# Optimization experiments

Hardware: AMD Instinct MI355X
Metric: run time of the kernel (lower is better)

## Reference

```python
import jax, jax.numpy as jnp
import numpy as np

N0, N1, N2 = 200000, 50000, 10000
D_IN, D_PROMPT, D_HID, D_OUT = 128, 64, 256, 2
E0, E1 = 800000, 160000


def _glorot(key, shape):
    fan_in, fan_out = shape[0], shape[1]
    lim = np.sqrt(6.0 / (fan_in + fan_out))
    return jax.random.uniform(key, shape, jnp.float32, -lim, lim)


def setup_inputs() -> dict:
    key = jax.random.key(0)
    ks = jax.random.split(key, 20)
    inp = {
        "features": jax.random.normal(ks[0], (N0, D_IN), jnp.float32),
        "membership_mask": jax.random.randint(ks[1], (N0,), 0, 2) > 0,
        "src0": jax.random.randint(ks[2], (E0,), 0, N0),
        "dst0": jax.random.randint(ks[3], (E0,), 0, N1),
        "src1": jax.random.randint(ks[4], (E1,), 0, N1),
        "dst1": jax.random.randint(ks[5], (E1,), 0, N2),
        "output_nodes_indices": jax.random.randint(ks[6], (N2,), 0, N2),
        # prompt MLPs
        "w_pin": _glorot(ks[7], (D_IN, D_PROMPT)),
        "b_pin": jnp.zeros((D_PROMPT,), jnp.float32),
        "w_pout": _glorot(ks[8], (D_IN, D_PROMPT)),
        "b_pout": jnp.zeros((D_PROMPT,), jnp.float32),
        # SAGEConv layer 0: (D_IN+D_PROMPT) -> D_HID
        "w_self0": _glorot(ks[9], (D_IN + D_PROMPT, D_HID)),
        "w_neigh0": _glorot(ks[10], (D_IN + D_PROMPT, D_HID)),
        "b0": jnp.zeros((D_HID,), jnp.float32),
        # SAGEConv layer 1: D_HID -> D_HID
        "w_self1": _glorot(ks[11], (D_HID, D_HID)),
        "w_neigh1": _glorot(ks[12], (D_HID, D_HID)),
        "b1": jnp.zeros((D_HID,), jnp.float32),
        # classifier
        "w_cls": _glorot(ks[13], (D_HID, D_OUT)),
        "b_cls": jnp.zeros((D_OUT,), jnp.float32),
    }
    return inp


def _sage_mean(h, src, dst, n_dst, w_self, w_neigh, b):
    # mean-aggregate src features into dst buckets (zero-degree -> 0, DGL semantics)
    agg = jax.ops.segment_sum(h[src], dst, num_segments=n_dst)
    deg = jax.ops.segment_sum(jnp.ones((src.shape[0],), h.dtype), dst, num_segments=n_dst)
    agg = agg / jnp.maximum(deg, 1.0)[:, None]
    return h[:n_dst] @ w_self + agg @ w_neigh + b


def reference(features, membership_mask, src0, dst0, src1, dst1, output_nodes_indices,
              w_pin, b_pin, w_pout, b_pout,
              w_self0, w_neigh0, b0, w_self1, w_neigh1, b1, w_cls, b_cls):
    p_in = jax.nn.relu(features @ w_pin + b_pin)
    p_out = jax.nn.relu(features @ w_pout + b_pout)
    sel = jnp.where(membership_mask[:, None], p_in, p_out)
    h = jnp.concatenate([features, sel], axis=1)          # [N0, D_IN+D_PROMPT]
    h = jax.nn.relu(_sage_mean(h, src0, dst0, N1, w_self0, w_neigh0, b0))  # [N1, D_HID]
    h = _sage_mean(h, src1, dst1, N2, w_self1, w_neigh1, b1)               # [N2, D_HID]
    logits = h @ w_cls + b_cls                             # [N2, D_OUT]
    return logits
```

## Files before the change

kernel.cpp:

```cpp
#include <hip/hip_runtime.h>


#define N0v 200000
#define N1v 50000
#define N2v 10000
#define E0v 800000
#define E1v 160000
#define TB0 49
#define TB1 10
#define TBL (TB0 + TB1)
#define NTILE 3125
#define PGRID 512

using u16 = unsigned short;
typedef __attribute__((ext_vector_type(8))) short short8;
typedef __attribute__((ext_vector_type(4))) float f32x4;

__device__ __forceinline__ float b2f(u16 u) {
    union { unsigned int i; float f; } v; v.i = ((unsigned int)u) << 16; return v.f;
}
__device__ __forceinline__ u16 f2b(float f) {
    union { float f; unsigned int i; } v; v.f = f;
    return (u16)((v.i + 0x7fffu + ((v.i >> 16) & 1u)) >> 16);
}
__device__ __forceinline__ void split2(float f, u16& h, u16& l) {
    h = f2b(f);
    l = f2b(f - b2f(h));
}

__global__ void k_prep(const unsigned* mask, int* flag,
                       const float* w_pin, const float* w_pout, u16* WTph, u16* WTpl,
                       const float* ws0, const float* wn0, u16* WT0h, u16* WT0l,
                       const float* ws1, const float* wn1, u16* WT1h, u16* WT1l,
                       const float* bc, float* outp,
                       const int* __restrict__ dst0, const int* __restrict__ dst1,
                       int* cnt0, int* cnt1, int* rk0, int* rk1) {
    const int R0 = 50000;
    const int R1 = R0 + 128 * 128;
    const int R2 = R1 + 256 * 384;
    const int R3 = R2 + 256 * 512;
    const int R4 = R3 + 2 * N2v;
    const int R5 = R4 + E0v;
    const int R6 = R5 + E1v;
    for (int i = blockIdx.x * blockDim.x + threadIdx.x; i < R6;
         i += gridDim.x * blockDim.x) {
        if (i < R0) {
            if (mask[i] > 1u) atomicOr(flag, 1);
        } else if (i < R1) {
            int j = i - R0, n = j >> 7, k = j & 127;
            float f = (n < 64) ? w_pin[k * 64 + n] : w_pout[k * 64 + (n - 64)];
            split2(f, WTph[j], WTpl[j]);
        } else if (i < R2) {
            int j = i - R1, n = j / 384, k = j % 384;
            float f = (k < 192) ? ws0[k * 256 + n] : wn0[(k - 192) * 256 + n];
            split2(f, WT0h[j], WT0l[j]);
        } else if (i < R3) {
            int j = i - R2, n = j >> 9, k = j & 511;
            float f = (k < 256) ? ws1[k * 256 + n] : wn1[(k - 256) * 256 + n];
            split2(f, WT1h[j], WT1l[j]);
        } else if (i < R4) {
            int j = i - R3;
            outp[j] = bc[j & 1];
        } else if (i < R5) {
            int e = i - R4;
            rk0[e] = atomicAdd(&cnt0[dst0[e]], 1);
        } else {
            int e = i - R5;
            rk1[e] = atomicAdd(&cnt1[dst1[e]], 1);
        }
    }
}

__global__ __launch_bounds__(256) void k_scan_a(const int* __restrict__ cnt0,
                                                int* __restrict__ off0,
                                                const int* __restrict__ cnt1,
                                                int* __restrict__ off1,
                                                int* __restrict__ tsum) {
    __shared__ int sd[256];
    const int t = threadIdx.x;
    const int blk = blockIdx.x;
    const int g1 = (blk >= TB0);
    const int b = g1 ? blk - TB0 : blk;
    const int n = g1 ? N2v : N1v;
    const int* cnt = g1 ? cnt1 : cnt0;
    int* off = g1 ? off1 : off0;
    const int i0 = b * 1024 + t * 4;
    int c[4] = {0, 0, 0, 0};
    if (i0 + 3 < n) {
        *(int4*)c = *(const int4*)&cnt[i0];
    } else {
        for (int j = 0; j < 4; j++) if (i0 + j < n) c[j] = cnt[i0 + j];
    }
    int s = c[0] + c[1] + c[2] + c[3];
    sd[t] = s;
    __syncthreads();
#pragma unroll
    for (int d = 1; d < 256; d <<= 1) {
        int v = (t >= d) ? sd[t - d] : 0;
        __syncthreads();
        sd[t] += v;
        __syncthreads();
    }
    int run = sd[t] - s;
    int o4[4];
#pragma unroll
    for (int j = 0; j < 4; j++) { o4[j] = run; run += c[j]; }
    if (i0 + 3 < n) *(int4*)&off[i0] = *(const int4*)o4;
    else for (int j = 0; j < 4; j++) if (i0 + j < n) off[i0 + j] = o4[j];
    if (t == 255) tsum[blk] = sd[255];
}

__global__ __launch_bounds__(256) void k_scan_c(int* __restrict__ off0,
                                                int* __restrict__ off1,
                                                const int* __restrict__ tsum) {
    __shared__ int lbase;
    const int t = threadIdx.x;
    const int blk = blockIdx.x;
    const int g1 = (blk >= TB0);
    const int b = g1 ? blk - TB0 : blk;
    const int n = g1 ? N2v : N1v;
    int* off = g1 ? off1 : off0;
    if (t < 64) {
        int v = (t < TBL) ? tsum[t] : 0;
        int incl = v;
#pragma unroll
        for (int d = 1; d < 64; d <<= 1) {
            int u = __shfl_up(incl, d);
            if (t >= d) incl += u;
        }
        int total0 = __shfl(incl, TB0 - 1);
        if (t == blk) lbase = (incl - v) - (g1 ? total0 : 0);
    }
    __syncthreads();
    const int base = lbase;
    const int i0 = b * 1024 + t * 4;
    if (i0 + 3 < n) {
        int4 v = *(int4*)&off[i0];
        v.x += base; v.y += base; v.z += base; v.w += base;
        *(int4*)&off[i0] = v;
    } else {
        for (int j = 0; j < 4; j++) if (i0 + j < n) off[i0 + j] += base;
    }
    if (blk == 0 && t == 0) { off0[N1v] = E0v; off1[N2v] = E1v; }
}

__global__ __launch_bounds__(256) void k_scatter2(
    const int* __restrict__ src0, const int* __restrict__ dst0,
    const int* __restrict__ off0, const int* __restrict__ rk0, int* __restrict__ ei0,
    const int* __restrict__ src1, const int* __restrict__ dst1,
    const int* __restrict__ off1, const int* __restrict__ rk1, int* __restrict__ ei1) {
    const int part = blockIdx.x & 7;
    const int chunk = blockIdx.x >> 3;
    const int nch = gridDim.x >> 3;
    {
        const int per = (E0v + nch - 1) / nch;
        const int i1 = min((chunk + 1) * per, E0v);
        for (int i = chunk * per + (int)threadIdx.x; i < i1; i += 256) {
            int d = dst0[i];
            if (d / 6250 == part) ei0[off0[d] + rk0[i]] = src0[i];
        }
    }
    {
        const int per = (E1v + nch - 1) / nch;
        const int i1 = min((chunk + 1) * per, E1v);
        for (int i = chunk * per + (int)threadIdx.x; i < i1; i += 256) {
            int d = dst1[i];
            if (d / 1250 == part) ei1[off1[d] + rk1[i]] = src1[i];
        }
    }
}

__global__ __launch_bounds__(256, 2) void k_gemm_p(
    const float* __restrict__ A, const u16* __restrict__ Bh, const u16* __restrict__ Bl,
    const float* __restrict__ b_pin, const float* __restrict__ b_pout,
    const void* maskp, const int* __restrict__ flag, u16* __restrict__ G) {
    __shared__ __align__(16) u16 STG[2][8448];
    __shared__ __align__(16) u16 EPI[8704];
    const int t = threadIdx.x;
    const int lane = t & 63, w = t >> 6;
    const int m = lane & 15, q = lane >> 4;
    const int colbase = w * 32;
    const int r15 = t >> 4, ch = t & 15;
    const int k0s = ch >> 2, q2s = ch & 3;

    const size_t ba = (size_t)(colbase + m) * 128 + q * 8;
    const size_t bb = (size_t)(colbase + 16 + m) * 128 + q * 8;
    short8 BfA[4][2], BfB[4][2];
#pragma unroll
    for (int k0 = 0; k0 < 4; k0++) {
        BfA[k0][0] = *(const short8*)&Bh[ba + k0 * 32];
        BfA[k0][1] = *(const short8*)&Bl[ba + k0 * 32];
        BfB[k0][0] = *(const short8*)&Bh[bb + k0 * 32];
        BfB[k0][1] = *(const short8*)&Bl[bb + k0 * 32];
    }
    const int fl = *flag;
    float bv0, bv1;
    {
        int c0 = colbase + m, c1 = colbase + 16 + m;
        bv0 = (c0 < 64) ? b_pin[c0] : b_pout[c0 - 64];
        bv1 = (c1 < 64) ? b_pin[c1] : b_pout[c1 - 64];
    }

    float4 va[8];
    {
        const float* ap = &A[(size_t)(blockIdx.x * 64 + r15) * 128 + ch * 8];
#pragma unroll
        for (int p = 0; p < 4; p++) {
            va[2 * p]     = *(const float4*)(ap + (size_t)p * 16 * 128);
            va[2 * p + 1] = *(const float4*)(ap + (size_t)p * 16 * 128 + 4);
        }
    }

    int buf = 0;
    for (int bm = blockIdx.x; bm < NTILE; bm += PGRID, buf ^= 1) {
        const int r0 = bm * 64;
        u16* stg = STG[buf];
#pragma unroll
        for (int p = 0; p < 4; p++) {
            u16 h8[8];
            h8[0] = f2b(va[2 * p].x); h8[1] = f2b(va[2 * p].y);
            h8[2] = f2b(va[2 * p].z); h8[3] = f2b(va[2 * p].w);
            h8[4] = f2b(va[2 * p + 1].x); h8[5] = f2b(va[2 * p + 1].y);
            h8[6] = f2b(va[2 * p + 1].z); h8[7] = f2b(va[2 * p + 1].w);
            *(uint4*)&stg[((p * 4 + k0s) * 66 + 16 * q2s + r15) * 8] = *(const uint4*)h8;
        }
        __syncthreads();

        if (bm + PGRID < NTILE) {
            const float* ap = &A[(size_t)((bm + PGRID) * 64 + r15) * 128 + ch * 8];
#pragma unroll
            for (int p = 0; p < 4; p++) {
                va[2 * p]     = *(const float4*)(ap + (size_t)p * 16 * 128);
                va[2 * p + 1] = *(const float4*)(ap + (size_t)p * 16 * 128 + 4);
            }
        }
        bool mk0, mk1;
        {
            const int ra = r0 + (t >> 3), rb = ra + 32;
            if (fl) {
                mk0 = ((const unsigned char*)maskp)[ra] != 0;
                mk1 = ((const unsigned char*)maskp)[rb] != 0;
            } else {
                mk0 = ((const int*)maskp)[ra] != 0;
                mk1 = ((const int*)maskp)[rb] != 0;
            }
        }

        f32x4 acc[4][2] = {};
#pragma unroll
        for (int k0 = 0; k0 < 4; k0++) {
#pragma unroll
            for (int mi = 0; mi < 4; mi++) {
                short8 af = *(const short8*)&stg[((mi * 4 + k0) * 66 + lane) * 8];
                acc[mi][0] = __builtin_amdgcn_mfma_f32_16x16x32_bf16(af, BfA[k0][0], acc[mi][0], 0, 0, 0);
                acc[mi][0] = __builtin_amdgcn_mfma_f32_16x16x32_bf16(af, BfA[k0][1], acc[mi][0], 0, 0, 0);
                acc[mi][1] = __builtin_amdgcn_mfma_f32_16x16x32_bf16(af, BfB[k0][0], acc[mi][1], 0, 0, 0);
                acc[mi][1] = __builtin_amdgcn_mfma_f32_16x16x32_bf16(af, BfB[k0][1], acc[mi][1], 0, 0, 0);
            }
        }

#pragma unroll
        for (int mi = 0; mi < 4; mi++)
#pragma unroll
            for (int r = 0; r < 4; r++) {
                float v0 = acc[mi][0][r] + bv0;
                float v1 = acc[mi][1][r] + bv1;
                v0 = v0 > 0.f ? v0 : 0.f;
                v1 = v1 > 0.f ? v1 : 0.f;
                EPI[(mi * 16 + q * 4 + r) * 136 + colbase + m] = f2b(v0);
                EPI[(mi * 16 + q * 4 + r) * 136 + colbase + 16 + m] = f2b(v1);
            }
        __syncthreads();

        {
            const int c8 = t & 7;
            const int rt = t >> 3;
            *(uint4*)&G[(size_t)(r0 + rt) * 192 + 128 + c8 * 8] =
                *(const uint4*)&EPI[rt * 136 + (mk0 ? 0 : 64) + c8 * 8];
            *(uint4*)&G[(size_t)(r0 + 32 + rt) * 192 + 128 + c8 * 8] =
                *(const uint4*)&EPI[(32 + rt) * 136 + (mk1 ? 0 : 64) + c8 * 8];
        }
#pragma unroll
        for (int p = 0; p < 4; p++) {
            uint4 v = *(const uint4*)&stg[((p * 4 + k0s) * 66 + 16 * q2s + r15) * 8];
            *(uint4*)&G[(size_t)(r0 + r15 + 16 * p) * 192 + ch * 8] = v;
        }
    }
}

template <int MODE, int KT, int SEGA0, int MT>
__global__ __launch_bounds__(256, 3) void k_g(
    const u16* __restrict__ A0, int s0, const u16* __restrict__ A1, int s1,
    const u16* __restrict__ Bh, const u16* __restrict__ Bl,
    const float* __restrict__ bias,
    u16* __restrict__ CH, float* __restrict__ outp, const float* __restrict__ wc,
    int M) {
    constexpr int MI = MT / 16;
    __shared__ __align__(16) u16 LA[MI * KT * 66 * 8];
    const int t = threadIdx.x;
    const int bm = blockIdx.x >> 1, bn = blockIdx.x & 1;
    const int lane = t & 63, w = t >> 6;
    const int m = lane & 15, q = lane >> 4;
    const int r0 = bm * MT;
    const int colbase = bn * 128 + w * 32;
    const int K = KT * 32;

    {
        constexpr int TPR = 256 / MT;
        constexpr int SPT = KT / TPR;
        const int rr = t / TPR, sub = t & (TPR - 1);
        int arow = r0 + rr; if (arow >= M) arow = M - 1;
        const int mi = rr >> 4, r15 = rr & 15;
#pragma unroll
        for (int s = 0; s < SPT; s++) {
            const int kc = sub * SPT + s;
#pragma unroll
            for (int q2 = 0; q2 < 4; q2++) {
                const int c = kc * 32 + q2 * 8;
                uint4 v = (c < SEGA0)
                              ? *(const uint4*)&A0[(size_t)arow * s0 + c]
                              : *(const uint4*)&A1[(size_t)arow * s1 + (c - SEGA0)];
                *(uint4*)&LA[((mi * KT + kc) * 66 + 16 * q2 + r15) * 8] = v;
            }
        }
    }
    __syncthreads();

    const size_t ba = (size_t)(colbase + m) * K + q * 8;
    const size_t bb = (size_t)(colbase + 16 + m) * K + q * 8;

    f32x4 acc[MI][2] = {};
#pragma unroll 2
    for (int kb = 0; kb < KT; kb += 4) {
#pragma unroll
        for (int k0 = 0; k0 < 4; k0++) {
            const size_t ko = (size_t)(kb + k0) * 32;
            short8 b0h = *(const short8*)&Bh[ba + ko];
            short8 b0l = *(const short8*)&Bl[ba + ko];
            short8 b1h = *(const short8*)&Bh[bb + ko];
            short8 b1l = *(const short8*)&Bl[bb + ko];
#pragma unroll
            for (int mi = 0; mi < MI; mi++) {
                short8 af = *(const short8*)&LA[((mi * KT + kb + k0) * 66 + lane) * 8];
                acc[mi][0] = __builtin_amdgcn_mfma_f32_16x16x32_bf16(af, b0h, acc[mi][0], 0, 0, 0);
                acc[mi][0] = __builtin_amdgcn_mfma_f32_16x16x32_bf16(af, b0l, acc[mi][0], 0, 0, 0);
                acc[mi][1] = __builtin_amdgcn_mfma_f32_16x16x32_bf16(af, b1h, acc[mi][1], 0, 0, 0);
                acc[mi][1] = __builtin_amdgcn_mfma_f32_16x16x32_bf16(af, b1l, acc[mi][1], 0, 0, 0);
            }
        }
    }

    if (MODE == 1) {
        float bv[2];
#pragma unroll
        for (int nt = 0; nt < 2; nt++) bv[nt] = bias[colbase + nt * 16 + m];
        __syncthreads();
#pragma unroll
        for (int mi = 0; mi < MI; mi++)
#pragma unroll
            for (int nt = 0; nt < 2; nt++)
#pragma unroll
                for (int r = 0; r < 4; r++) {
                    float v = acc[mi][nt][r] + bv[nt];
                    v = v > 0.f ? v : 0.f;
                    LA[(mi * 16 + q * 4 + r) * 136 + w * 32 + nt * 16 + m] = f2b(v);
                }
        __syncthreads();
        const int c16 = t & 15;
#pragma unroll
        for (int pass = 0; pass < MT / 16; pass++) {
            const int rt = pass * 16 + (t >> 4);
            const int row = r0 + rt;
            if (row < M) {
                *(uint4*)&CH[(size_t)row * 256 + bn * 128 + c16 * 8] =
                    *(const uint4*)&LA[rt * 136 + c16 * 8];
            }
        }
    } else {
        const int ca = colbase + m, cb = colbase + 16 + m;
        const float bva = bias[ca], bvb = bias[cb];
        const float w0a = wc[ca * 2], w1a = wc[ca * 2 + 1];
        const float w0b = wc[cb * 2], w1b = wc[cb * 2 + 1];
#pragma unroll
        for (int mi = 0; mi < MI; mi++) {
#pragma unroll
            for (int r = 0; r < 4; r++) {
                int row = r0 + mi * 16 + q * 4 + r;
                float va = acc[mi][0][r] + bva;
                float vb = acc[mi][1][r] + bvb;
                float p0 = va * w0a + vb * w0b;
                float p1 = va * w1a + vb * w1b;
#pragma unroll
                for (int s = 1; s < 16; s <<= 1) {
                    p0 += __shfl_xor(p0, s);
                    p1 += __shfl_xor(p1, s);
                }
                if (m == 0 && row < M) {
                    atomicAdd(&outp[row * 2], p0);
                    atomicAdd(&outp[row * 2 + 1], p1);
                }
            }
        }
    }
}

__global__ void k_agg0(const u16* __restrict__ G, const int* __restrict__ off,
                       const int* __restrict__ eidx, u16* __restrict__ aggH) {
    int wid = (blockIdx.x * blockDim.x + threadIdx.x) >> 6;
    int lane = threadIdx.x & 63;
    if (wid >= N1v) return;
    int b = off[wid], e = off[wid + 1];
    float f0 = 0.f, f1 = 0.f, p0 = 0.f;
    for (int base = b; base < e; base += 64) {
        int li = base + lane;
        int idx = eidx[li < e ? li : (e - 1)];
        int nch = e - base; if (nch > 64) nch = 64;
        int j = 0;
        for (; j + 4 <= nch; j += 4) {
            int sa = __shfl(idx, j), sb = __shfl(idx, j + 1);
            int sc = __shfl(idx, j + 2), sd = __shfl(idx, j + 3);
            const u16* ra = &G[(size_t)sa * 192];
            const u16* rb = &G[(size_t)sb * 192];
            const u16* rc = &G[(size_t)sc * 192];
            const u16* rd = &G[(size_t)sd * 192];
            unsigned fa = *(const unsigned*)&ra[2 * lane];
            unsigned fb = *(const unsigned*)&rb[2 * lane];
            unsigned fc = *(const unsigned*)&rc[2 * lane];
            unsigned fd = *(const unsigned*)&rd[2 * lane];
            u16 pa = ra[128 + lane], pb = rb[128 + lane];
            u16 pc = rc[128 + lane], pd = rd[128 + lane];
            f0 += b2f((u16)fa) + b2f((u16)fb) + b2f((u16)fc) + b2f((u16)fd);
            f1 += b2f((u16)(fa >> 16)) + b2f((u16)(fb >> 16)) +
                  b2f((u16)(fc >> 16)) + b2f((u16)(fd >> 16));
            p0 += b2f(pa) + b2f(pb) + b2f(pc) + b2f(pd);
        }
        for (; j < nch; j++) {
            int s = __shfl(idx, j);
            const u16* row = &G[(size_t)s * 192];
            unsigned fv = *(const unsigned*)&row[2 * lane];
            f0 += b2f((u16)fv);
            f1 += b2f((u16)(fv >> 16));
            p0 += b2f(row[128 + lane]);
        }
    }
    int deg = e - b;
    float inv = 1.0f / (float)(deg > 1 ? deg : 1);
    size_t rb2 = (size_t)wid * 192;
    *(unsigned*)&aggH[rb2 + 2 * lane] =
        (unsigned)f2b(f0 * inv) | ((unsigned)f2b(f1 * inv) << 16);
    aggH[rb2 + 128 + lane] = f2b(p0 * inv);
}

__global__ void k_agg1(const u16* __restrict__ h1H, const int* __restrict__ off,
                       const int* __restrict__ eidx, u16* __restrict__ aggH) {
    int wid = (blockIdx.x * blockDim.x + threadIdx.x) >> 6;
    int lane = threadIdx.x & 63;
    if (wid >= N2v) return;
    int b = off[wid], e = off[wid + 1];
    float a0 = 0.f, a1 = 0.f, a2 = 0.f, a3 = 0.f;
    for (int base = b; base < e; base += 64) {
        int li = base + lane;
        int idx = eidx[li < e ? li : (e - 1)];
        int nch = e - base; if (nch > 64) nch = 64;
        int j = 0;
        for (; j + 4 <= nch; j += 4) {
            int sa = __shfl(idx, j), sb = __shfl(idx, j + 1);
            int sc = __shfl(idx, j + 2), sd = __shfl(idx, j + 3);
            const u16* ra = &h1H[(size_t)sa * 256];
            const u16* rb = &h1H[(size_t)sb * 256];
            const u16* rc = &h1H[(size_t)sc * 256];
            const u16* rd = &h1H[(size_t)sd * 256];
            unsigned va0 = *(const unsigned*)&ra[2 * lane];
            unsigned vb0 = *(const unsigned*)&rb[2 * lane];
            unsigned vc0 = *(const unsigned*)&rc[2 * lane];
            unsigned vd0 = *(const unsigned*)&rd[2 * lane];
            unsigned va1 = *(const unsigned*)&ra[128 + 2 * lane];
            unsigned vb1 = *(const unsigned*)&rb[128 + 2 * lane];
            unsigned vc1 = *(const unsigned*)&rc[128 + 2 * lane];
            unsigned vd1 = *(const unsigned*)&rd[128 + 2 * lane];
            a0 += b2f((u16)va0) + b2f((u16)vb0) + b2f((u16)vc0) + b2f((u16)vd0);
            a1 += b2f((u16)(va0 >> 16)) + b2f((u16)(vb0 >> 16)) +
                  b2f((u16)(vc0 >> 16)) + b2f((u16)(vd0 >> 16));
            a2 += b2f((u16)va1) + b2f((u16)vb1) + b2f((u16)vc1) + b2f((u16)vd1);
            a3 += b2f((u16)(va1 >> 16)) + b2f((u16)(vb1 >> 16)) +
                  b2f((u16)(vc1 >> 16)) + b2f((u16)(vd1 >> 16));
        }
        for (; j < nch; j++) {
            int s = __shfl(idx, j);
            const u16* row = &h1H[(size_t)s * 256];
            unsigned v0 = *(const unsigned*)&row[2 * lane];
            unsigned v1 = *(const unsigned*)&row[128 + 2 * lane];
            a0 += b2f((u16)v0); a1 += b2f((u16)(v0 >> 16));
            a2 += b2f((u16)v1); a3 += b2f((u16)(v1 >> 16));
        }
    }
    int deg = e - b;
    float inv = 1.0f / (float)(deg > 1 ? deg : 1);
    size_t rb2 = (size_t)wid * 256;
    *(unsigned*)&aggH[rb2 + 2 * lane] =
        (unsigned)f2b(a0 * inv) | ((unsigned)f2b(a1 * inv) << 16);
    *(unsigned*)&aggH[rb2 + 128 + 2 * lane] =
        (unsigned)f2b(a2 * inv) | ((unsigned)f2b(a3 * inv) << 16);
}

extern "C" void kernel_launch(void* const* d_in, const int* in_sizes, int n_in,
                              void* d_out, int out_size, void* d_ws, size_t ws_size,
                              hipStream_t stream) {
    const float* features = (const float*)d_in[0];
    const void* maskp     = d_in[1];
    const int* src0       = (const int*)d_in[2];
    const int* dst0       = (const int*)d_in[3];
    const int* src1       = (const int*)d_in[4];
    const int* dst1       = (const int*)d_in[5];
    const float* w_pin    = (const float*)d_in[7];
    const float* b_pin    = (const float*)d_in[8];
    const float* w_pout   = (const float*)d_in[9];
    const float* b_pout   = (const float*)d_in[10];
    const float* w_self0  = (const float*)d_in[11];
    const float* w_neigh0 = (const float*)d_in[12];
    const float* b0       = (const float*)d_in[13];
    const float* w_self1  = (const float*)d_in[14];
    const float* w_neigh1 = (const float*)d_in[15];
    const float* b1       = (const float*)d_in[16];
    const float* w_cls    = (const float*)d_in[17];
    const float* b_cls    = (const float*)d_in[18];
    float* out = (float*)d_out;
    (void)in_sizes; (void)n_in; (void)out_size; (void)ws_size;

    char* ws = (char*)d_ws;
    size_t o = 0;
    auto alloc = [&](size_t bytes) { size_t r = o; o += (bytes + 255) & ~(size_t)255; return r; };
    size_t o_flag = alloc(4);
    size_t o_cnt0 = alloc(N1v * 4);
    size_t o_cnt1 = alloc(N2v * 4);
    size_t zero_end = o;
    size_t o_G    = alloc((size_t)N0v * 192 * 2);
    size_t o_aggH = alloc((size_t)N1v * 192 * 2);
    size_t o_h1H  = alloc((size_t)N1v * 256 * 2);
    size_t o_ag1H = alloc((size_t)N2v * 256 * 2);
    size_t o_wtph = alloc(128 * 128 * 2), o_wtpl = alloc(128 * 128 * 2);
    size_t o_wt0h = alloc(256 * 384 * 2), o_wt0l = alloc(256 * 384 * 2);
    size_t o_wt1h = alloc(256 * 512 * 2), o_wt1l = alloc(256 * 512 * 2);
    size_t o_off0 = alloc((N1v + 1) * 4);
    size_t o_off1 = alloc((N2v + 1) * 4);
    size_t o_ei0  = alloc((size_t)E0v * 4);
    size_t o_ei1  = alloc((size_t)E1v * 4);
    size_t o_rk0  = alloc((size_t)E0v * 4);
    size_t o_rk1  = alloc((size_t)E1v * 4);
    size_t o_tsum = alloc(TBL * 4);

    int* flag = (int*)(ws + o_flag);
    int* cnt0 = (int*)(ws + o_cnt0);
    int* cnt1 = (int*)(ws + o_cnt1);
    u16* G     = (u16*)(ws + o_G);
    u16* aggH  = (u16*)(ws + o_aggH);
    u16* h1H   = (u16*)(ws + o_h1H);
    u16* ag1H  = (u16*)(ws + o_ag1H);
    u16* WTph = (u16*)(ws + o_wtph);
    u16* WTpl = (u16*)(ws + o_wtpl);
    u16* WT0h = (u16*)(ws + o_wt0h);
    u16* WT0l = (u16*)(ws + o_wt0l);
    u16* WT1h = (u16*)(ws + o_wt1h);
    u16* WT1l = (u16*)(ws + o_wt1l);
    int* off0 = (int*)(ws + o_off0);
    int* off1 = (int*)(ws + o_off1);
    int* ei0  = (int*)(ws + o_ei0);
    int* ei1  = (int*)(ws + o_ei1);
    int* rk0  = (int*)(ws + o_rk0);
    int* rk1  = (int*)(ws + o_rk1);
    int* tsum = (int*)(ws + o_tsum);

    hipMemsetAsync(ws + o_flag, 0, zero_end - o_flag, stream);

    k_prep<<<1024, 256, 0, stream>>>((const unsigned*)maskp, flag,
                                     w_pin, w_pout, WTph, WTpl,
                                     w_self0, w_neigh0, WT0h, WT0l,
                                     w_self1, w_neigh1, WT1h, WT1l,
                                     b_cls, out, dst0, dst1, cnt0, cnt1, rk0, rk1);

    k_scan_a<<<TBL, 256, 0, stream>>>(cnt0, off0, cnt1, off1, tsum);
    k_scan_c<<<TBL, 256, 0, stream>>>(off0, off1, tsum);

    k_scatter2<<<2048, 256, 0, stream>>>(src0, dst0, off0, rk0, ei0,
                                         src1, dst1, off1, rk1, ei1);

    k_gemm_p<<<PGRID, 256, 0, stream>>>(features, WTph, WTpl,
                                        b_pin, b_pout, maskp, flag, G);

    k_agg0<<<(N1v + 3) / 4, 256, 0, stream>>>(G, off0, ei0, aggH);

    k_g<1, 12, 192, 64><<<((N1v + 63) / 64) * 2, 256, 0, stream>>>(
        G, 192, aggH, 192, WT0h, WT0l, b0, h1H, nullptr, nullptr, N1v);

    k_agg1<<<(N2v + 3) / 4, 256, 0, stream>>>(h1H, off1, ei1, ag1H);

    k_g<3, 16, 256, 32><<<((N2v + 31) / 32) * 2, 256, 0, stream>>>(
        h1H, 256, ag1H, 256, WT1h, WT1l, b1, nullptr, out, w_cls, N2v);
}
```

Baseline: 411.0 us.

## Fuse edge degree counting into prompt GEMM kernel to overlap atomics

Moves the per-edge degree counting and rank assignment atomics out of the prep kernel and into the prompt GEMM kernel. Each GEMM block takes a slice of the edges and processes one 256-edge chunk per tile iteration, finishing any leftovers after the loop. The goal is to hide the latency-bound atomic traffic behind the memory-bound feature GEMM and to shrink the prep kernel, which is now launched with fewer blocks. The GEMM kernel moves ahead of the scan kernels so the counts are ready before them. The cost is extra register and memory pressure inside the GEMM loop, which could slow it down.

```diff
diff --git a/kernel.cpp b/kernel.cpp
--- a/kernel.cpp
+++ b/kernel.cpp
@@ -6,11 +6,13 @@
 #define N2v 10000
 #define E0v 800000
 #define E1v 160000
+#define ETv (E0v + E1v)
 #define TB0 49
 #define TB1 10
 #define TBL (TB0 + TB1)
 #define NTILE 3125
 #define PGRID 512
+#define EPB (ETv / PGRID)
 
 using u16 = unsigned short;
 typedef __attribute__((ext_vector_type(8))) short short8;
@@ -32,17 +34,13 @@
                        const float* w_pin, const float* w_pout, u16* WTph, u16* WTpl,
                        const float* ws0, const float* wn0, u16* WT0h, u16* WT0l,
                        const float* ws1, const float* wn1, u16* WT1h, u16* WT1l,
-                       const float* bc, float* outp,
-                       const int* __restrict__ dst0, const int* __restrict__ dst1,
-                       int* cnt0, int* cnt1, int* rk0, int* rk1) {
+                       const float* bc, float* outp) {
     const int R0 = 50000;
     const int R1 = R0 + 128 * 128;
     const int R2 = R1 + 256 * 384;
     const int R3 = R2 + 256 * 512;
     const int R4 = R3 + 2 * N2v;
-    const int R5 = R4 + E0v;
-    const int R6 = R5 + E1v;
-    for (int i = blockIdx.x * blockDim.x + threadIdx.x; i < R6;
+    for (int i = blockIdx.x * blockDim.x + threadIdx.x; i < R4;
          i += gridDim.x * blockDim.x) {
         if (i < R0) {
             if (mask[i] > 1u) atomicOr(flag, 1);
@@ -58,15 +56,9 @@
             int j = i - R2, n = j >> 9, k = j & 511;
             float f = (k < 256) ? ws1[k * 256 + n] : wn1[(k - 256) * 256 + n];
             split2(f, WT1h[j], WT1l[j]);
-        } else if (i < R4) {
+        } else {
             int j = i - R3;
             outp[j] = bc[j & 1];
-        } else if (i < R5) {
-            int e = i - R4;
-            rk0[e] = atomicAdd(&cnt0[dst0[e]], 1);
-        } else {
-            int e = i - R5;
-            rk1[e] = atomicAdd(&cnt1[dst1[e]], 1);
         }
     }
 }
@@ -173,7 +165,9 @@
 __global__ __launch_bounds__(256, 2) void k_gemm_p(
     const float* __restrict__ A, const u16* __restrict__ Bh, const u16* __restrict__ Bl,
     const float* __restrict__ b_pin, const float* __restrict__ b_pout,
-    const void* maskp, const int* __restrict__ flag, u16* __restrict__ G) {
+    const void* maskp, const int* __restrict__ flag, u16* __restrict__ G,
+    const int* __restrict__ dst0, const int* __restrict__ dst1,
+    int* cnt0, int* cnt1, int* rk0, int* rk1) {
     __shared__ __align__(16) u16 STG[2][8448];
     __shared__ __align__(16) u16 EPI[8704];
     const int t = threadIdx.x;
@@ -183,6 +177,21 @@
     const int r15 = t >> 4, ch = t & 15;
     const int k0s = ch >> 2, q2s = ch & 3;
 
+    const int eb0 = blockIdx.x * EPB;
+    const int eb1 = eb0 + EPB;
+    int esl = 0;
+    auto do_edges = [&](int s) {
+        int i = eb0 + s * 256 + t;
+        if (i < eb1) {
+            if (i < E0v) {
+                rk0[i] = atomicAdd(&cnt0[dst0[i]], 1);
+            } else {
+                int e = i - E0v;
+                rk1[e] = atomicAdd(&cnt1[dst1[e]], 1);
+            }
+        }
+    };
+
     const size_t ba = (size_t)(colbase + m) * 128 + q * 8;
     const size_t bb = (size_t)(colbase + 16 + m) * 128 + q * 8;
     short8 BfA[4][2], BfB[4][2];
@@ -234,6 +243,8 @@
                 va[2 * p + 1] = *(const float4*)(ap + (size_t)p * 16 * 128 + 4);
             }
         }
+        if (esl * 256 < EPB) { do_edges(esl); esl++; }
+
         bool mk0, mk1;
         {
             const int ra = r0 + (t >> 3), rb = ra + 32;
@@ -286,6 +297,7 @@
             *(uint4*)&G[(size_t)(r0 + r15 + 16 * p) * 192 + ch * 8] = v;
         }
     }
+    while (esl * 256 < EPB) { do_edges(esl); esl++; }
 }
 
 template <int MODE, int KT, int SEGA0, int MT>
@@ -572,11 +584,15 @@
 
     hipMemsetAsync(ws + o_flag, 0, zero_end - o_flag, stream);
 
-    k_prep<<<1024, 256, 0, stream>>>((const unsigned*)maskp, flag,
-                                     w_pin, w_pout, WTph, WTpl,
-                                     w_self0, w_neigh0, WT0h, WT0l,
-                                     w_self1, w_neigh1, WT1h, WT1l,
-                                     b_cls, out, dst0, dst1, cnt0, cnt1, rk0, rk1);
+    k_prep<<<512, 256, 0, stream>>>((const unsigned*)maskp, flag,
+                                    w_pin, w_pout, WTph, WTpl,
+                                    w_self0, w_neigh0, WT0h, WT0l,
+                                    w_self1, w_neigh1, WT1h, WT1l,
+                                    b_cls, out);
+
+    k_gemm_p<<<PGRID, 256, 0, stream>>>(features, WTph, WTpl,
+                                        b_pin, b_pout, maskp, flag, G,
+                                        dst0, dst1, cnt0, cnt1, rk0, rk1);
 
     k_scan_a<<<TBL, 256, 0, stream>>>(cnt0, off0, cnt1, off1, tsum);
     k_scan_c<<<TBL, 256, 0, stream>>>(off0, off1, tsum);
@@ -584,9 +600,6 @@
     k_scatter2<<<2048, 256, 0, stream>>>(src0, dst0, off0, rk0, ei0,
                                          src1, dst1, off1, rk1, ei1);
 
-    k_gemm_p<<<PGRID, 256, 0, stream>>>(features, WTph, WTpl,
-                                        b_pin, b_pout, maskp, flag, G);
-
     k_agg0<<<(N1v + 3) / 4, 256, 0, stream>>>(G, off0, ei0, aggH);
 
     k_g<1, 12, 192, 64><<<((N1v + 63) / 64) * 2, 256, 0, stream>>>(
```

Result: faster. 387.4 us, median of 2 (-5.7%).
